# Performance work log

Measured on AMD Instinct MI355X. Metric: run time of the kernel, lower is better.

Reference implementation:

```python
import jax, jax.numpy as jnp
import numpy as np

B, N, D, C = 128, 512, 1024, 512  # batch, prune_hidden, out_dim, context_dim


def setup_inputs() -> dict:
    key = jax.random.key(0)
    ks = jax.random.split(key, 6)
    s = jax.random.normal(ks[0], (B, N + D), jnp.float32)
    context = jax.random.normal(ks[1], (B, C), jnp.float32)
    Wa = jax.random.normal(ks[2], (N, N), jnp.float32) / np.sqrt(N).astype(np.float32)
    Wc = jax.random.normal(ks[3], (C, N), jnp.float32) / np.sqrt(C).astype(np.float32)
    ba = jnp.zeros((N,), jnp.float32)
    Wl = jax.random.normal(ks[4], (N, D), jnp.float32) / np.sqrt(N).astype(np.float32)
    bl = jnp.zeros((D,), jnp.float32)
    t = jnp.float32(0.5)
    return {"t": t, "s": s, "context": context, "Wa": Wa, "Wc": Wc,
            "ba": ba, "Wl": Wl, "bl": bl}


def reference(t, s, context, Wa, Wc, ba, Wl, bl):
    # split augmented state: a = Koopman latent, z = observable channel
    n = Wa.shape[0]
    a = s[:, :n]          # (B, N)
    z = s[:, n:]          # (B, D)

    # a_ode(t, a, context): context-conditioned latent drift (stand-in for M.a_ode)
    da = jnp.tanh(a @ Wa + context @ Wc + ba)          # (B, N)

    # c = M.a_ode.lat2out(a): linear readout to observable dim
    c = a @ Wl + bl                                    # (B, D)

    # circulant_matrix[:, i, :] = roll(c, shifts=i, dims=1)
    # => circ[b, i, j] = c[b, (j - i) % D]; built via one gather instead of a D-loop
    d = c.shape[1]
    idx = (jnp.arange(d)[None, :] - jnp.arange(d)[:, None]) % d   # (D, D)
    circ = c[:, idx]                                   # (B, D, D)

    # dz = bmm(circ, z[:, :, None]).squeeze(-1)
    dz = jnp.einsum('bij,bj->bi', circ, z)             # (B, D)

    return jnp.concatenate([da, dz], axis=-1)          # (B, N + D)
```

## Files before the change

### kernel.cpp

```cpp
#include <hip/hip_runtime.h>
#include <math.h>


typedef float f32x4 __attribute__((ext_vector_type(4)));
typedef float f32x2 __attribute__((ext_vector_type(2)));
typedef float f32x4v __attribute__((ext_vector_type(4)));
typedef __bf16 bf16x8 __attribute__((ext_vector_type(8)));
typedef __bf16 bf16x4 __attribute__((ext_vector_type(4)));

#define C_OFF_BYTES 262144

__device__ __forceinline__ bf16x8 pack2(float4 v0, float4 v1) {
    bf16x8 r;
    r[0] = (__bf16)v0.x; r[1] = (__bf16)v0.y; r[2] = (__bf16)v0.z; r[3] = (__bf16)v0.w;
    r[4] = (__bf16)v1.x; r[5] = (__bf16)v1.y; r[6] = (__bf16)v1.z; r[7] = (__bf16)v1.w;
    return r;
}

__device__ __forceinline__ uint2 cvt4(float4 v) {
    bf16x4 r;
    r[0] = (__bf16)v.x; r[1] = (__bf16)v.y; r[2] = (__bf16)v.z; r[3] = (__bf16)v.w;
    return __builtin_bit_cast(uint2, r);
}

__device__ __forceinline__ unsigned short bf16u(float f) {
    return __builtin_bit_cast(unsigned short, (__bf16)f);
}

__device__ __forceinline__ f32x4 MFMA(uint4 a, uint4 b, f32x4 c) {
    return __builtin_amdgcn_mfma_f32_16x16x32_bf16(
        __builtin_bit_cast(bf16x8, a), __builtin_bit_cast(bf16x8, b), c, 0, 0, 0);
}

__global__ __launch_bounds__(512) void k1(
    const float* __restrict__ s, const float* __restrict__ ctx,
    const float* __restrict__ Wl, const float* __restrict__ bl,
    unsigned short* __restrict__ ws16, float* __restrict__ cws)
{
    __shared__ __align__(16) unsigned char smem[56832];

    const int bid = blockIdx.x;
    const int t = threadIdx.x;
    const int w = t >> 6, l = t & 63;
    const int lk = l & 15, kq = l >> 4;

    if (bid < 256) {
        const int mt = bid >> 6, nt = bid & 63;
        const int col = nt * 16 + lk;
        const int N0 = nt * 16;
        unsigned short* Abuf = reinterpret_cast<unsigned short*>(smem);
        unsigned short* Bbuf = reinterpret_cast<unsigned short*>(smem + 32768);
        float* red = reinterpret_cast<float*>(smem + 49152);

        {
            const int q = t & 3;
            const int r0 = t >> 2;
            #pragma unroll 4
            for (int p = 0; p < 4; ++p) {
                const int k = r0 + 128 * p;
                float4 v = *reinterpret_cast<const float4*>(
                    Wl + (size_t)k * 1024 + N0 + 4 * q);
                const int ks = k >> 5, kr = k & 31;
                const int kqs = (kr & 15) >> 2;
                const int jj = (kr & 3) + 4 * (kr >> 4);
                const int base = (ks * 64 + 16 * kqs + 4 * q) * 8 + jj;
                Bbuf[base]      = bf16u(v.x);
                Bbuf[base + 8]  = bf16u(v.y);
                Bbuf[base + 16] = bf16u(v.z);
                Bbuf[base + 24] = bf16u(v.w);
            }
        }

        {
            const int r = t >> 4;
            const int wmA = r >> 4, lkA = r & 15;
            const float* src = s + (size_t)(mt * 32 + r) * 1536;
            #pragma unroll 8
            for (int rep = 0; rep < 8; ++rep) {
                const int q = (t & 15) + 16 * rep;
                float4 v = *reinterpret_cast<const float4*>(src + 4 * q);
                const int ksA = q >> 3, kqA = q & 3, half = (q >> 2) & 1;
                const int off = ((wmA * 16 + ksA) * 64 + kqA * 16 + lkA) * 8 + half * 4;
                *reinterpret_cast<uint2*>(&Abuf[off]) = cvt4(v);
            }
        }
        __syncthreads();

        const int wm = w & 1, wk = w >> 1;
        f32x4 acc0 = (f32x4){0.f, 0.f, 0.f, 0.f};
        f32x4 acc1 = (f32x4){0.f, 0.f, 0.f, 0.f};
        #pragma unroll 4
        for (int i = 0; i < 4; ++i) {
            const int ks = wk * 4 + i;
            uint4 av = *reinterpret_cast<const uint4*>(&Abuf[((wm * 16 + ks) * 64 + l) * 8]);
            uint4 bv = *reinterpret_cast<const uint4*>(&Bbuf[(ks * 64 + l) * 8]);
            if (i & 1) acc1 = MFMA(av, bv, acc1);
            else       acc0 = MFMA(av, bv, acc0);
        }
        f32x4 sum = acc0 + acc1;

        if (wk > 0) {
            #pragma unroll
            for (int r = 0; r < 4; ++r)
                red[((wk - 1) * 32 + wm * 16 + 4 * kq + r) * 20 + lk] = sum[r];
        }
        __syncthreads();
        if (wk == 0) {
            const float bias = bl[col];
            #pragma unroll
            for (int r = 0; r < 4; ++r) {
                const int m = wm * 16 + 4 * kq + r;
                float v = sum[r] + red[m * 20 + lk] + red[(32 + m) * 20 + lk]
                        + red[(64 + m) * 20 + lk] + bias;
                cws[(size_t)(mt * 32 + m) * 1024 + col] = v;
            }
        }
    } else {
        const int base = (bid - 256) * 512 + t;
        #pragma unroll 2
        for (int rep = 0; rep < 2; ++rep) {
            const int idx = base + rep * 8192;
            const int mt = idx >> 11, ks = (idx >> 6) & 31, l2 = idx & 63;
            const int lk2 = l2 & 15, kq2 = l2 >> 4;
            const int row = 16 * mt + lk2, kb = 32 * ks;
            float4 v0, v1;
            if (ks < 16) {
                v0 = *reinterpret_cast<const float4*>(s + (size_t)row * 1536 + kb + 4 * kq2);
                v1 = *reinterpret_cast<const float4*>(s + (size_t)row * 1536 + kb + 16 + 4 * kq2);
            } else {
                v0 = *reinterpret_cast<const float4*>(ctx + (size_t)row * 512 + (kb - 512) + 4 * kq2);
                v1 = *reinterpret_cast<const float4*>(ctx + (size_t)row * 512 + (kb - 512) + 16 + 4 * kq2);
            }
            bf16x8 fr = pack2(v0, v1);
            *reinterpret_cast<uint4*>(ws16 + (size_t)idx * 8) = __builtin_bit_cast(uint4, fr);
        }
    }
}

__global__ __launch_bounds__(512) void k2(
    const float* __restrict__ s,
    const float* __restrict__ Wa, const float* __restrict__ Wc,
    const float* __restrict__ ba,
    const unsigned short* __restrict__ apack, const float* __restrict__ cws,
    float* __restrict__ out)
{
    __shared__ __align__(16) unsigned char smem[37888];

    const int bid = blockIdx.x;
    const int t = threadIdx.x;

    if (bid < 256) {
        float* zdup = reinterpret_cast<float*>(smem);
        float* zsh  = reinterpret_cast<float*>(smem + 8256);
        float* part = reinterpret_cast<float*>(smem + 16464);
        const int b = bid >> 1;
        const int I0 = (bid & 1) * 512;
        const float* zrow = s + (size_t)b * 1536 + 512;

        if (t < 256) {
            float4 v = reinterpret_cast<const float4*>(zrow)[t];
            reinterpret_cast<float4*>(zdup)[t] = v;
            reinterpret_cast<float4*>(zdup)[256 + t] = v;
        } else if (t == 256) {
            reinterpret_cast<float4*>(zdup)[512] = reinterpret_cast<const float4*>(zrow)[0];
        }
        __syncthreads();
        {
            f32x4v v0 = reinterpret_cast<const f32x4v*>(zdup)[t];
            f32x4v v1 = reinterpret_cast<const f32x4v*>(zdup)[t + 1];
            f32x4v r = {v0.y, v0.z, v0.w, v1.x};
            reinterpret_cast<f32x4v*>(zsh)[t] = r;
        }
        __syncthreads();

        const int g = t & 63;
        const int kq = __builtin_amdgcn_readfirstlane(t >> 6);
        const int i0 = 8 * g;
        const int koff = kq * 128;
        const int eb = (I0 + i0 + koff) >> 2;

        const f32x4v* zE = reinterpret_cast<const f32x4v*>(zdup);
        const f32x4v* zO = reinterpret_cast<const f32x4v*>(zsh);
        const f32x4v* c4 = reinterpret_cast<const f32x4v*>(cws + (size_t)b * 1024 + koff);

        f32x4v e0 = zE[eb], e1 = zE[eb + 1];
        f32x4v o0 = zO[eb], o1 = zO[eb + 1];
        f32x2 acc[8];
        #pragma unroll
        for (int q = 0; q < 8; ++q) acc[q] = (f32x2){0.f, 0.f};

        #pragma unroll 8
        for (int p2 = 0; p2 < 32; ++p2) {
            f32x4v cf = c4[p2];
            f32x4v e2 = zE[eb + p2 + 2];
            f32x4v o2 = zO[eb + p2 + 2];
            f32x2 cA = cf.lo, cB = cf.hi;
            acc[0] = __builtin_elementwise_fma(cA, e0.lo, acc[0]);
            acc[1] = __builtin_elementwise_fma(cA, o0.lo, acc[1]);
            acc[2] = __builtin_elementwise_fma(cA, e0.hi, acc[2]);
            acc[3] = __builtin_elementwise_fma(cA, o0.hi, acc[3]);
            acc[4] = __builtin_elementwise_fma(cA, e1.lo, acc[4]);
            acc[5] = __builtin_elementwise_fma(cA, o1.lo, acc[5]);
            acc[6] = __builtin_elementwise_fma(cA, e1.hi, acc[6]);
            acc[7] = __builtin_elementwise_fma(cA, o1.hi, acc[7]);
            acc[0] = __builtin_elementwise_fma(cB, e0.hi, acc[0]);
            acc[1] = __builtin_elementwise_fma(cB, o0.hi, acc[1]);
            acc[2] = __builtin_elementwise_fma(cB, e1.lo, acc[2]);
            acc[3] = __builtin_elementwise_fma(cB, o1.lo, acc[3]);
            acc[4] = __builtin_elementwise_fma(cB, e1.hi, acc[4]);
            acc[5] = __builtin_elementwise_fma(cB, o1.hi, acc[5]);
            acc[6] = __builtin_elementwise_fma(cB, e2.lo, acc[6]);
            acc[7] = __builtin_elementwise_fma(cB, o2.lo, acc[7]);
            e0 = e1; e1 = e2; o0 = o1; o1 = o2;
        }

        float4 r0, r1;
        r0.x = acc[0].x + acc[0].y; r0.y = acc[1].x + acc[1].y;
        r0.z = acc[2].x + acc[2].y; r0.w = acc[3].x + acc[3].y;
        r1.x = acc[4].x + acc[4].y; r1.y = acc[5].x + acc[5].y;
        r1.z = acc[6].x + acc[6].y; r1.w = acc[7].x + acc[7].y;
        reinterpret_cast<float4*>(&part[kq * 512 + i0])[0] = r0;
        reinterpret_cast<float4*>(&part[kq * 512 + i0])[1] = r1;
        __syncthreads();
        float sumz = 0.f;
        #pragma unroll
        for (int q = 0; q < 8; ++q) sumz += part[q * 512 + t];
        out[(size_t)b * 1536 + 512 + I0 + t] = sumz;
    } else {
        unsigned short* Bg = reinterpret_cast<unsigned short*>(smem);
        float* red = reinterpret_cast<float*>(smem + 32768);
        const int j = bid - 256;
        const int mt = j >> 5, nt = j & 31;
        const int w = t >> 6, l = t & 63;
        const int lk = l & 15, kq = l >> 4;
        const int col = nt * 16 + lk;

        #pragma unroll 4
        for (int i = 0; i < 4; ++i) {
            const int ks = w * 4 + i;
            const int kb = ks * 32;
            const float* wb; int krel;
            if (ks < 16) { wb = Wa; krel = kb; } else { wb = Wc; krel = kb - 512; }
            bf16x8 fr;
            #pragma unroll
            for (int jj = 0; jj < 4; ++jj)
                fr[jj] = (__bf16)wb[(size_t)(krel + 4 * kq + jj) * 512 + col];
            #pragma unroll
            for (int jj = 0; jj < 4; ++jj)
                fr[4 + jj] = (__bf16)wb[(size_t)(krel + 16 + 4 * kq + jj) * 512 + col];
            *reinterpret_cast<uint4*>(&Bg[(ks * 64 + l) * 8]) = __builtin_bit_cast(uint4, fr);
        }
        __syncthreads();

        f32x4 acc0 = (f32x4){0.f, 0.f, 0.f, 0.f};
        f32x4 acc1 = (f32x4){0.f, 0.f, 0.f, 0.f};
        #pragma unroll 4
        for (int i = 0; i < 4; ++i) {
            const int ks = w * 4 + i;
            uint4 av = *reinterpret_cast<const uint4*>(apack + ((size_t)(mt * 32 + ks) * 64 + l) * 8);
            uint4 bv = *reinterpret_cast<const uint4*>(&Bg[(ks * 64 + l) * 8]);
            if (i & 1) acc1 = MFMA(av, bv, acc1);
            else       acc0 = MFMA(av, bv, acc0);
        }
        f32x4 sum = acc0 + acc1;

        if (w < 4) {
            #pragma unroll
            for (int r = 0; r < 4; ++r)
                red[w * 272 + (kq * 4 + r) * 17 + lk] = sum[r];
        }
        __syncthreads();
        if (w >= 4) {
            #pragma unroll
            for (int r = 0; r < 4; ++r)
                red[(w - 4) * 272 + (kq * 4 + r) * 17 + lk] += sum[r];
        }
        __syncthreads();
        if (t < 256) {
            const int m = t >> 4, n = t & 15;
            const int o = m * 17 + n;
            const int colo = nt * 16 + n;
            float v = red[o] + red[272 + o] + red[544 + o] + red[816 + o] + ba[colo];
            out[(size_t)(mt * 16 + m) * 1536 + colo] = tanhf(v);
        }
    }
}

extern "C" void kernel_launch(void* const* d_in, const int* in_sizes, int n_in,
                              void* d_out, int out_size, void* d_ws, size_t ws_size,
                              hipStream_t stream) {
    const float* s   = (const float*)d_in[1];
    const float* ctx = (const float*)d_in[2];
    const float* Wa  = (const float*)d_in[3];
    const float* Wc  = (const float*)d_in[4];
    const float* ba  = (const float*)d_in[5];
    const float* Wl  = (const float*)d_in[6];
    const float* bl  = (const float*)d_in[7];
    float* out = (float*)d_out;

    unsigned short* ws16 = (unsigned short*)d_ws;
    float* cws = (float*)((char*)d_ws + C_OFF_BYTES);

    k1<<<272, 512, 0, stream>>>(s, ctx, Wl, bl, ws16, cws);
    k2<<<512, 512, 0, stream>>>(s, Wa, Wc, ba, ws16, cws, out);
}
```

Baseline: 14.55 us.

## Move tanh GEMM into first kernel and drop global bf16 A prepack

The da = tanh(a@Wa + ctx@Wc + ba) GEMM blocks move from the second kernel into the first, which already computes c = a@Wl + bl. They now convert their A tile straight from s/ctx into shared memory instead of reading a bf16 prepack from workspace. The second kernel keeps only the circulant dz blocks. This removes the prepack pass and its global round trip and shortens the dependent second launch. In exchange the first kernel grows to 512 blocks with about 70KB of shared memory, which may lower occupancy, and each GEMM block re-converts its A tile itself.

Measured after the change: 15.02 us. 3.3% more time.

```diff
diff --git a/kernel.cpp b/kernel.cpp
--- a/kernel.cpp
+++ b/kernel.cpp
@@ -8,15 +8,6 @@
 typedef __bf16 bf16x8 __attribute__((ext_vector_type(8)));
 typedef __bf16 bf16x4 __attribute__((ext_vector_type(4)));
 
-#define C_OFF_BYTES 262144
-
-__device__ __forceinline__ bf16x8 pack2(float4 v0, float4 v1) {
-    bf16x8 r;
-    r[0] = (__bf16)v0.x; r[1] = (__bf16)v0.y; r[2] = (__bf16)v0.z; r[3] = (__bf16)v0.w;
-    r[4] = (__bf16)v1.x; r[5] = (__bf16)v1.y; r[6] = (__bf16)v1.z; r[7] = (__bf16)v1.w;
-    return r;
-}
-
 __device__ __forceinline__ uint2 cvt4(float4 v) {
     bf16x4 r;
     r[0] = (__bf16)v.x; r[1] = (__bf16)v.y; r[2] = (__bf16)v.z; r[3] = (__bf16)v.w;
@@ -34,10 +25,12 @@
 
 __global__ __launch_bounds__(512) void k1(
     const float* __restrict__ s, const float* __restrict__ ctx,
-    const float* __restrict__ Wl, const float* __restrict__ bl,
-    unsigned short* __restrict__ ws16, float* __restrict__ cws)
+    const float* __restrict__ Wa, const float* __restrict__ Wc,
+    const float* __restrict__ ba, const float* __restrict__ Wl,
+    const float* __restrict__ bl, float* __restrict__ out,
+    float* __restrict__ cws)
 {
-    __shared__ __align__(16) unsigned char smem[56832];
+    __shared__ __align__(16) unsigned char smem[69888];
 
     const int bid = blockIdx.x;
     const int t = threadIdx.x;
@@ -70,16 +63,15 @@
                 Bbuf[base + 24] = bf16u(v.w);
             }
         }
-
         {
             const int r = t >> 4;
-            const int wmA = r >> 4, lkA = r & 15;
             const float* src = s + (size_t)(mt * 32 + r) * 1536;
             #pragma unroll 8
             for (int rep = 0; rep < 8; ++rep) {
                 const int q = (t & 15) + 16 * rep;
                 float4 v = *reinterpret_cast<const float4*>(src + 4 * q);
                 const int ksA = q >> 3, kqA = q & 3, half = (q >> 2) & 1;
+                const int wmA = r >> 4, lkA = r & 15;
                 const int off = ((wmA * 16 + ksA) * 64 + kqA * 16 + lkA) * 8 + half * 4;
                 *reinterpret_cast<uint2*>(&Abuf[off]) = cvt4(v);
             }
@@ -116,123 +108,11 @@
             }
         }
     } else {
-        const int base = (bid - 256) * 512 + t;
-        #pragma unroll 2
-        for (int rep = 0; rep < 2; ++rep) {
-            const int idx = base + rep * 8192;
-            const int mt = idx >> 11, ks = (idx >> 6) & 31, l2 = idx & 63;
-            const int lk2 = l2 & 15, kq2 = l2 >> 4;
-            const int row = 16 * mt + lk2, kb = 32 * ks;
-            float4 v0, v1;
-            if (ks < 16) {
-                v0 = *reinterpret_cast<const float4*>(s + (size_t)row * 1536 + kb + 4 * kq2);
-                v1 = *reinterpret_cast<const float4*>(s + (size_t)row * 1536 + kb + 16 + 4 * kq2);
-            } else {
-                v0 = *reinterpret_cast<const float4*>(ctx + (size_t)row * 512 + (kb - 512) + 4 * kq2);
-                v1 = *reinterpret_cast<const float4*>(ctx + (size_t)row * 512 + (kb - 512) + 16 + 4 * kq2);
-            }
-            bf16x8 fr = pack2(v0, v1);
-            *reinterpret_cast<uint4*>(ws16 + (size_t)idx * 8) = __builtin_bit_cast(uint4, fr);
-        }
-    }
-}
-
-__global__ __launch_bounds__(512) void k2(
-    const float* __restrict__ s,
-    const float* __restrict__ Wa, const float* __restrict__ Wc,
-    const float* __restrict__ ba,
-    const unsigned short* __restrict__ apack, const float* __restrict__ cws,
-    float* __restrict__ out)
-{
-    __shared__ __align__(16) unsigned char smem[37888];
-
-    const int bid = blockIdx.x;
-    const int t = threadIdx.x;
-
-    if (bid < 256) {
-        float* zdup = reinterpret_cast<float*>(smem);
-        float* zsh  = reinterpret_cast<float*>(smem + 8256);
-        float* part = reinterpret_cast<float*>(smem + 16464);
-        const int b = bid >> 1;
-        const int I0 = (bid & 1) * 512;
-        const float* zrow = s + (size_t)b * 1536 + 512;
-
-        if (t < 256) {
-            float4 v = reinterpret_cast<const float4*>(zrow)[t];
-            reinterpret_cast<float4*>(zdup)[t] = v;
-            reinterpret_cast<float4*>(zdup)[256 + t] = v;
-        } else if (t == 256) {
-            reinterpret_cast<float4*>(zdup)[512] = reinterpret_cast<const float4*>(zrow)[0];
-        }
-        __syncthreads();
-        {
-            f32x4v v0 = reinterpret_cast<const f32x4v*>(zdup)[t];
-            f32x4v v1 = reinterpret_cast<const f32x4v*>(zdup)[t + 1];
-            f32x4v r = {v0.y, v0.z, v0.w, v1.x};
-            reinterpret_cast<f32x4v*>(zsh)[t] = r;
-        }
-        __syncthreads();
-
-        const int g = t & 63;
-        const int kq = __builtin_amdgcn_readfirstlane(t >> 6);
-        const int i0 = 8 * g;
-        const int koff = kq * 128;
-        const int eb = (I0 + i0 + koff) >> 2;
-
-        const f32x4v* zE = reinterpret_cast<const f32x4v*>(zdup);
-        const f32x4v* zO = reinterpret_cast<const f32x4v*>(zsh);
-        const f32x4v* c4 = reinterpret_cast<const f32x4v*>(cws + (size_t)b * 1024 + koff);
-
-        f32x4v e0 = zE[eb], e1 = zE[eb + 1];
-        f32x4v o0 = zO[eb], o1 = zO[eb + 1];
-        f32x2 acc[8];
-        #pragma unroll
-        for (int q = 0; q < 8; ++q) acc[q] = (f32x2){0.f, 0.f};
-
-        #pragma unroll 8
-        for (int p2 = 0; p2 < 32; ++p2) {
-            f32x4v cf = c4[p2];
-            f32x4v e2 = zE[eb + p2 + 2];
-            f32x4v o2 = zO[eb + p2 + 2];
-            f32x2 cA = cf.lo, cB = cf.hi;
-            acc[0] = __builtin_elementwise_fma(cA, e0.lo, acc[0]);
-            acc[1] = __builtin_elementwise_fma(cA, o0.lo, acc[1]);
-            acc[2] = __builtin_elementwise_fma(cA, e0.hi, acc[2]);
-            acc[3] = __builtin_elementwise_fma(cA, o0.hi, acc[3]);
-            acc[4] = __builtin_elementwise_fma(cA, e1.lo, acc[4]);
-            acc[5] = __builtin_elementwise_fma(cA, o1.lo, acc[5]);
-            acc[6] = __builtin_elementwise_fma(cA, e1.hi, acc[6]);
-            acc[7] = __builtin_elementwise_fma(cA, o1.hi, acc[7]);
-            acc[0] = __builtin_elementwise_fma(cB, e0.hi, acc[0]);
-            acc[1] = __builtin_elementwise_fma(cB, o0.hi, acc[1]);
-            acc[2] = __builtin_elementwise_fma(cB, e1.lo, acc[2]);
-            acc[3] = __builtin_elementwise_fma(cB, o1.lo, acc[3]);
-            acc[4] = __builtin_elementwise_fma(cB, e1.hi, acc[4]);
-            acc[5] = __builtin_elementwise_fma(cB, o1.hi, acc[5]);
-            acc[6] = __builtin_elementwise_fma(cB, e2.lo, acc[6]);
-            acc[7] = __builtin_elementwise_fma(cB, o2.lo, acc[7]);
-            e0 = e1; e1 = e2; o0 = o1; o1 = o2;
-        }
-
-        float4 r0, r1;
-        r0.x = acc[0].x + acc[0].y; r0.y = acc[1].x + acc[1].y;
-        r0.z = acc[2].x + acc[2].y; r0.w = acc[3].x + acc[3].y;
-        r1.x = acc[4].x + acc[4].y; r1.y = acc[5].x + acc[5].y;
-        r1.z = acc[6].x + acc[6].y; r1.w = acc[7].x + acc[7].y;
-        reinterpret_cast<float4*>(&part[kq * 512 + i0])[0] = r0;
-        reinterpret_cast<float4*>(&part[kq * 512 + i0])[1] = r1;
-        __syncthreads();
-        float sumz = 0.f;
-        #pragma unroll
-        for (int q = 0; q < 8; ++q) sumz += part[q * 512 + t];
-        out[(size_t)b * 1536 + 512 + I0 + t] = sumz;
-    } else {
-        unsigned short* Bg = reinterpret_cast<unsigned short*>(smem);
-        float* red = reinterpret_cast<float*>(smem + 32768);
+        unsigned short* Abuf = reinterpret_cast<unsigned short*>(smem);
+        unsigned short* Bg = reinterpret_cast<unsigned short*>(smem + 32768);
+        float* red = reinterpret_cast<float*>(smem + 65536);
         const int j = bid - 256;
         const int mt = j >> 5, nt = j & 31;
-        const int w = t >> 6, l = t & 63;
-        const int lk = l & 15, kq = l >> 4;
         const int col = nt * 16 + lk;
 
         #pragma unroll 4
@@ -250,6 +130,21 @@
                 fr[4 + jj] = (__bf16)wb[(size_t)(krel + 16 + 4 * kq + jj) * 512 + col];
             *reinterpret_cast<uint4*>(&Bg[(ks * 64 + l) * 8]) = __builtin_bit_cast(uint4, fr);
         }
+        {
+            const int r = t >> 5;
+            const float* srow = s + (size_t)(16 * mt + r) * 1536;
+            const float* crow = ctx + (size_t)(16 * mt + r) * 512;
+            #pragma unroll 8
+            for (int rep = 0; rep < 8; ++rep) {
+                const int q = (t & 31) + 32 * rep;
+                float4 v;
+                if (rep < 4) v = *reinterpret_cast<const float4*>(srow + 4 * q);
+                else         v = *reinterpret_cast<const float4*>(crow + 4 * q - 512);
+                const int ksA = q >> 3, kqA = q & 3, half = (q >> 2) & 1;
+                const int off = (ksA * 64 + kqA * 16 + r) * 8 + half * 4;
+                *reinterpret_cast<uint2*>(&Abuf[off]) = cvt4(v);
+            }
+        }
         __syncthreads();
 
         f32x4 acc0 = (f32x4){0.f, 0.f, 0.f, 0.f};
@@ -257,7 +152,7 @@
         #pragma unroll 4
         for (int i = 0; i < 4; ++i) {
             const int ks = w * 4 + i;
-            uint4 av = *reinterpret_cast<const uint4*>(apack + ((size_t)(mt * 32 + ks) * 64 + l) * 8);
+            uint4 av = *reinterpret_cast<const uint4*>(&Abuf[(ks * 64 + l) * 8]);
             uint4 bv = *reinterpret_cast<const uint4*>(&Bg[(ks * 64 + l) * 8]);
             if (i & 1) acc1 = MFMA(av, bv, acc1);
             else       acc0 = MFMA(av, bv, acc0);
@@ -284,6 +179,91 @@
             out[(size_t)(mt * 16 + m) * 1536 + colo] = tanhf(v);
         }
     }
+}
+
+__global__ __launch_bounds__(512) void k2(const float* __restrict__ s,
+                                          const float* __restrict__ cws,
+                                          float* __restrict__ out)
+{
+    __shared__ __align__(16) unsigned char smem[33024];
+    float* zdup = reinterpret_cast<float*>(smem);
+    float* zsh  = reinterpret_cast<float*>(smem + 8256);
+    float* part = reinterpret_cast<float*>(smem + 16464);
+    const int bid = blockIdx.x;
+    const int t = threadIdx.x;
+    const int b = bid >> 1;
+    const int I0 = (bid & 1) * 512;
+    const float* zrow = s + (size_t)b * 1536 + 512;
+
+    if (t < 256) {
+        float4 v = reinterpret_cast<const float4*>(zrow)[t];
+        reinterpret_cast<float4*>(zdup)[t] = v;
+        reinterpret_cast<float4*>(zdup)[256 + t] = v;
+    } else if (t == 256) {
+        reinterpret_cast<float4*>(zdup)[512] = reinterpret_cast<const float4*>(zrow)[0];
+    }
+    __syncthreads();
+    {
+        f32x4v v0 = reinterpret_cast<const f32x4v*>(zdup)[t];
+        f32x4v v1 = reinterpret_cast<const f32x4v*>(zdup)[t + 1];
+        f32x4v r = {v0.y, v0.z, v0.w, v1.x};
+        reinterpret_cast<f32x4v*>(zsh)[t] = r;
+    }
+    __syncthreads();
+
+    const int g = t & 63;
+    const int kq = __builtin_amdgcn_readfirstlane(t >> 6);
+    const int i0 = 8 * g;
+    const int koff = kq * 128;
+    const int eb = (I0 + i0 + koff) >> 2;
+
+    const f32x4v* zE = reinterpret_cast<const f32x4v*>(zdup);
+    const f32x4v* zO = reinterpret_cast<const f32x4v*>(zsh);
+    const f32x4v* c4 = reinterpret_cast<const f32x4v*>(cws + (size_t)b * 1024 + koff);
+
+    f32x4v e0 = zE[eb], e1 = zE[eb + 1];
+    f32x4v o0 = zO[eb], o1 = zO[eb + 1];
+    f32x2 acc[8];
+    #pragma unroll
+    for (int q = 0; q < 8; ++q) acc[q] = (f32x2){0.f, 0.f};
+
+    #pragma unroll 8
+    for (int p2 = 0; p2 < 32; ++p2) {
+        f32x4v cf = c4[p2];
+        f32x4v e2 = zE[eb + p2 + 2];
+        f32x4v o2 = zO[eb + p2 + 2];
+        f32x2 cA = cf.lo, cB = cf.hi;
+        acc[0] = __builtin_elementwise_fma(cA, e0.lo, acc[0]);
+        acc[1] = __builtin_elementwise_fma(cA, o0.lo, acc[1]);
+        acc[2] = __builtin_elementwise_fma(cA, e0.hi, acc[2]);
+        acc[3] = __builtin_elementwise_fma(cA, o0.hi, acc[3]);
+        acc[4] = __builtin_elementwise_fma(cA, e1.lo, acc[4]);
+        acc[5] = __builtin_elementwise_fma(cA, o1.lo, acc[5]);
+        acc[6] = __builtin_elementwise_fma(cA, e1.hi, acc[6]);
+        acc[7] = __builtin_elementwise_fma(cA, o1.hi, acc[7]);
+        acc[0] = __builtin_elementwise_fma(cB, e0.hi, acc[0]);
+        acc[1] = __builtin_elementwise_fma(cB, o0.hi, acc[1]);
+        acc[2] = __builtin_elementwise_fma(cB, e1.lo, acc[2]);
+        acc[3] = __builtin_elementwise_fma(cB, o1.lo, acc[3]);
+        acc[4] = __builtin_elementwise_fma(cB, e1.hi, acc[4]);
+        acc[5] = __builtin_elementwise_fma(cB, o1.hi, acc[5]);
+        acc[6] = __builtin_elementwise_fma(cB, e2.lo, acc[6]);
+        acc[7] = __builtin_elementwise_fma(cB, o2.lo, acc[7]);
+        e0 = e1; e1 = e2; o0 = o1; o1 = o2;
+    }
+
+    float4 r0, r1;
+    r0.x = acc[0].x + acc[0].y; r0.y = acc[1].x + acc[1].y;
+    r0.z = acc[2].x + acc[2].y; r0.w = acc[3].x + acc[3].y;
+    r1.x = acc[4].x + acc[4].y; r1.y = acc[5].x + acc[5].y;
+    r1.z = acc[6].x + acc[6].y; r1.w = acc[7].x + acc[7].y;
+    reinterpret_cast<float4*>(&part[kq * 512 + i0])[0] = r0;
+    reinterpret_cast<float4*>(&part[kq * 512 + i0])[1] = r1;
+    __syncthreads();
+    float sumz = 0.f;
+    #pragma unroll
+    for (int q = 0; q < 8; ++q) sumz += part[q * 512 + t];
+    out[(size_t)b * 1536 + 512 + I0 + t] = sumz;
 }
 
 extern "C" void kernel_launch(void* const* d_in, const int* in_sizes, int n_in,
@@ -297,10 +277,8 @@
     const float* Wl  = (const float*)d_in[6];
     const float* bl  = (const float*)d_in[7];
     float* out = (float*)d_out;
-
-    unsigned short* ws16 = (unsigned short*)d_ws;
-    float* cws = (float*)((char*)d_ws + C_OFF_BYTES);
-
-    k1<<<272, 512, 0, stream>>>(s, ctx, Wl, bl, ws16, cws);
-    k2<<<512, 512, 0, stream>>>(s, Wa, Wc, ba, ws16, cws, out);
-}
+    float* cws = (float*)d_ws;
+
+    k1<<<512, 512, 0, stream>>>(s, ctx, Wa, Wc, ba, Wl, bl, out, cws);
+    k2<<<256, 512, 0, stream>>>(s, cws, out);
+}
```

## Split k1 GEMM into 16-row tiles and fold pack work into every block

Applied to the files above, without the earlier changes.

The first kernel now launches 512 blocks, each computing a 16x16 output tile of c = a@Wl. Previously 256 GEMM blocks computed 32x16 tiles and 16 extra blocks did the bf16 packing of the activations. The packing is now spread across all blocks, 32 threads each, and the K-split reduction uses a two-stage shared-memory add. This is meant to fill more CUs and balance load on a small problem. In exchange, every block reloads its Wl slice, doubling Wl reads, and adds an extra barrier.

Result: slower. 14.91 us (+2.5%).

```diff
diff --git a/kernel.cpp b/kernel.cpp
--- a/kernel.cpp
+++ b/kernel.cpp
@@ -37,103 +37,99 @@
     const float* __restrict__ Wl, const float* __restrict__ bl,
     unsigned short* __restrict__ ws16, float* __restrict__ cws)
 {
-    __shared__ __align__(16) unsigned char smem[56832];
+    __shared__ __align__(16) unsigned char smem[37120];
 
     const int bid = blockIdx.x;
     const int t = threadIdx.x;
     const int w = t >> 6, l = t & 63;
     const int lk = l & 15, kq = l >> 4;
 
-    if (bid < 256) {
-        const int mt = bid >> 6, nt = bid & 63;
-        const int col = nt * 16 + lk;
-        const int N0 = nt * 16;
-        unsigned short* Abuf = reinterpret_cast<unsigned short*>(smem);
-        unsigned short* Bbuf = reinterpret_cast<unsigned short*>(smem + 32768);
-        float* red = reinterpret_cast<float*>(smem + 49152);
-
-        {
-            const int q = t & 3;
-            const int r0 = t >> 2;
-            #pragma unroll 4
-            for (int p = 0; p < 4; ++p) {
-                const int k = r0 + 128 * p;
-                float4 v = *reinterpret_cast<const float4*>(
-                    Wl + (size_t)k * 1024 + N0 + 4 * q);
-                const int ks = k >> 5, kr = k & 31;
-                const int kqs = (kr & 15) >> 2;
-                const int jj = (kr & 3) + 4 * (kr >> 4);
-                const int base = (ks * 64 + 16 * kqs + 4 * q) * 8 + jj;
-                Bbuf[base]      = bf16u(v.x);
-                Bbuf[base + 8]  = bf16u(v.y);
-                Bbuf[base + 16] = bf16u(v.z);
-                Bbuf[base + 24] = bf16u(v.w);
-            }
-        }
-
-        {
-            const int r = t >> 4;
-            const int wmA = r >> 4, lkA = r & 15;
-            const float* src = s + (size_t)(mt * 32 + r) * 1536;
-            #pragma unroll 8
-            for (int rep = 0; rep < 8; ++rep) {
-                const int q = (t & 15) + 16 * rep;
-                float4 v = *reinterpret_cast<const float4*>(src + 4 * q);
-                const int ksA = q >> 3, kqA = q & 3, half = (q >> 2) & 1;
-                const int off = ((wmA * 16 + ksA) * 64 + kqA * 16 + lkA) * 8 + half * 4;
-                *reinterpret_cast<uint2*>(&Abuf[off]) = cvt4(v);
-            }
-        }
-        __syncthreads();
-
-        const int wm = w & 1, wk = w >> 1;
-        f32x4 acc0 = (f32x4){0.f, 0.f, 0.f, 0.f};
-        f32x4 acc1 = (f32x4){0.f, 0.f, 0.f, 0.f};
+    if (t < 32) {
+        const int idx = bid * 32 + t;
+        const int mtA = idx >> 11, ksA = (idx >> 6) & 31, l2 = idx & 63;
+        const int lk2 = l2 & 15, kq2 = l2 >> 4;
+        const int row = 16 * mtA + lk2, kb = 32 * ksA;
+        float4 v0, v1;
+        if (ksA < 16) {
+            v0 = *reinterpret_cast<const float4*>(s + (size_t)row * 1536 + kb + 4 * kq2);
+            v1 = *reinterpret_cast<const float4*>(s + (size_t)row * 1536 + kb + 16 + 4 * kq2);
+        } else {
+            v0 = *reinterpret_cast<const float4*>(ctx + (size_t)row * 512 + (kb - 512) + 4 * kq2);
+            v1 = *reinterpret_cast<const float4*>(ctx + (size_t)row * 512 + (kb - 512) + 16 + 4 * kq2);
+        }
+        bf16x8 fr = pack2(v0, v1);
+        *reinterpret_cast<uint4*>(ws16 + (size_t)idx * 8) = __builtin_bit_cast(uint4, fr);
+    }
+
+    const int mt = bid >> 6;
+    const int nt = bid & 63;
+    const int N0 = nt * 16;
+    unsigned short* Abuf = reinterpret_cast<unsigned short*>(smem);
+    unsigned short* Bbuf = reinterpret_cast<unsigned short*>(smem + 16384);
+    float* red = reinterpret_cast<float*>(smem + 32768);
+
+    {
+        const int q = t & 3;
+        const int r0 = t >> 2;
         #pragma unroll 4
-        for (int i = 0; i < 4; ++i) {
-            const int ks = wk * 4 + i;
-            uint4 av = *reinterpret_cast<const uint4*>(&Abuf[((wm * 16 + ks) * 64 + l) * 8]);
-            uint4 bv = *reinterpret_cast<const uint4*>(&Bbuf[(ks * 64 + l) * 8]);
-            if (i & 1) acc1 = MFMA(av, bv, acc1);
-            else       acc0 = MFMA(av, bv, acc0);
-        }
-        f32x4 sum = acc0 + acc1;
-
-        if (wk > 0) {
-            #pragma unroll
-            for (int r = 0; r < 4; ++r)
-                red[((wk - 1) * 32 + wm * 16 + 4 * kq + r) * 20 + lk] = sum[r];
-        }
-        __syncthreads();
-        if (wk == 0) {
-            const float bias = bl[col];
-            #pragma unroll
-            for (int r = 0; r < 4; ++r) {
-                const int m = wm * 16 + 4 * kq + r;
-                float v = sum[r] + red[m * 20 + lk] + red[(32 + m) * 20 + lk]
-                        + red[(64 + m) * 20 + lk] + bias;
-                cws[(size_t)(mt * 32 + m) * 1024 + col] = v;
-            }
-        }
-    } else {
-        const int base = (bid - 256) * 512 + t;
-        #pragma unroll 2
-        for (int rep = 0; rep < 2; ++rep) {
-            const int idx = base + rep * 8192;
-            const int mt = idx >> 11, ks = (idx >> 6) & 31, l2 = idx & 63;
-            const int lk2 = l2 & 15, kq2 = l2 >> 4;
-            const int row = 16 * mt + lk2, kb = 32 * ks;
-            float4 v0, v1;
-            if (ks < 16) {
-                v0 = *reinterpret_cast<const float4*>(s + (size_t)row * 1536 + kb + 4 * kq2);
-                v1 = *reinterpret_cast<const float4*>(s + (size_t)row * 1536 + kb + 16 + 4 * kq2);
-            } else {
-                v0 = *reinterpret_cast<const float4*>(ctx + (size_t)row * 512 + (kb - 512) + 4 * kq2);
-                v1 = *reinterpret_cast<const float4*>(ctx + (size_t)row * 512 + (kb - 512) + 16 + 4 * kq2);
-            }
-            bf16x8 fr = pack2(v0, v1);
-            *reinterpret_cast<uint4*>(ws16 + (size_t)idx * 8) = __builtin_bit_cast(uint4, fr);
-        }
+        for (int p = 0; p < 4; ++p) {
+            const int k = r0 + 128 * p;
+            float4 v = *reinterpret_cast<const float4*>(
+                Wl + (size_t)k * 1024 + N0 + 4 * q);
+            const int ks = k >> 5, kr = k & 31;
+            const int kqs = (kr & 15) >> 2;
+            const int jj = (kr & 3) + 4 * (kr >> 4);
+            const int base = (ks * 64 + 16 * kqs + 4 * q) * 8 + jj;
+            Bbuf[base]      = bf16u(v.x);
+            Bbuf[base + 8]  = bf16u(v.y);
+            Bbuf[base + 16] = bf16u(v.z);
+            Bbuf[base + 24] = bf16u(v.w);
+        }
+    }
+    {
+        const int r = t >> 5;
+        const float* src = s + (size_t)(16 * mt + r) * 1536;
+        #pragma unroll 4
+        for (int rep = 0; rep < 4; ++rep) {
+            const int q = (t & 31) + 32 * rep;
+            float4 v = *reinterpret_cast<const float4*>(src + 4 * q);
+            const int ksA = q >> 3, kqA = q & 3, half = (q >> 2) & 1;
+            const int off = (ksA * 64 + kqA * 16 + r) * 8 + half * 4;
+            *reinterpret_cast<uint2*>(&Abuf[off]) = cvt4(v);
+        }
+    }
+    __syncthreads();
+
+    f32x4 acc0 = (f32x4){0.f, 0.f, 0.f, 0.f};
+    f32x4 acc1 = (f32x4){0.f, 0.f, 0.f, 0.f};
+    {
+        const int ks0 = 2 * w;
+        uint4 av0 = *reinterpret_cast<const uint4*>(&Abuf[(ks0 * 64 + l) * 8]);
+        uint4 bv0 = *reinterpret_cast<const uint4*>(&Bbuf[(ks0 * 64 + l) * 8]);
+        acc0 = MFMA(av0, bv0, acc0);
+        uint4 av1 = *reinterpret_cast<const uint4*>(&Abuf[((ks0 + 1) * 64 + l) * 8]);
+        uint4 bv1 = *reinterpret_cast<const uint4*>(&Bbuf[((ks0 + 1) * 64 + l) * 8]);
+        acc1 = MFMA(av1, bv1, acc1);
+    }
+    f32x4 sum = acc0 + acc1;
+
+    if (w < 4) {
+        #pragma unroll
+        for (int r = 0; r < 4; ++r)
+            red[w * 272 + (kq * 4 + r) * 17 + lk] = sum[r];
+    }
+    __syncthreads();
+    if (w >= 4) {
+        #pragma unroll
+        for (int r = 0; r < 4; ++r)
+            red[(w - 4) * 272 + (kq * 4 + r) * 17 + lk] += sum[r];
+    }
+    __syncthreads();
+    if (t < 256) {
+        const int m = t >> 4, n = t & 15;
+        const int o = m * 17 + n;
+        float v = red[o] + red[272 + o] + red[544 + o] + red[816 + o] + bl[N0 + n];
+        cws[(size_t)(16 * mt + m) * 1024 + N0 + n] = v;
     }
 }
 
@@ -301,6 +297,6 @@
     unsigned short* ws16 = (unsigned short*)d_ws;
     float* cws = (float*)((char*)d_ws + C_OFF_BYTES);
 
-    k1<<<272, 512, 0, stream>>>(s, ctx, Wl, bl, ws16, cws);
+    k1<<<512, 512, 0, stream>>>(s, ctx, Wl, bl, ws16, cws);
     k2<<<512, 512, 0, stream>>>(s, Wa, Wc, ba, ws16, cws, out);
 }
```
